# Optimization experiments

Hardware: AMD Instinct MI355X
Metric: run time of the kernel (lower is better)

Reference implementation:

```python
import jax, jax.numpy as jnp
import numpy as np

D_HEAD = 128
H_Q = 16
H_K = 4
D_MODEL = 2048
B = 2
T = 2048


def setup_inputs() -> dict:
    key = jax.random.key(0)
    k1, k2, k3, k4, k5 = jax.random.split(key, 5)
    s = 0.02
    return {
        "x": jax.random.normal(k1, (B, T, D_MODEL), dtype=jnp.float32),
        "wq": jax.random.normal(k2, (D_HEAD * H_Q, D_MODEL), dtype=jnp.float32) * s,
        "wk": jax.random.normal(k3, (D_HEAD * H_K, D_MODEL), dtype=jnp.float32) * s,
        "wv": jax.random.normal(k4, (D_HEAD * H_K, D_MODEL), dtype=jnp.float32) * s,
        "wo": jax.random.normal(k5, (D_MODEL, D_HEAD * H_Q), dtype=jnp.float32) * s,
    }


def reference(x, wq, wk, wv, wo):
    Bs, Ts, _ = x.shape
    g = H_Q // H_K  # query groups per kv head
    # projections (torch Linear: y = x @ W^T)
    Q = (x @ wq.T).reshape(Bs, Ts, H_Q, D_HEAD).transpose(0, 2, 1, 3)  # [B,hq,T,d]
    K = (x @ wk.T).reshape(Bs, Ts, H_K, D_HEAD).transpose(0, 2, 1, 3)  # [B,hk,T,d]
    V = (x @ wv.T).reshape(Bs, Ts, H_K, D_HEAD).transpose(0, 2, 1, 3)  # [B,hk,T,d]
    Qg = Q.reshape(Bs, g, H_K, Ts, D_HEAD)  # [B,g,hk,T,d]
    scale = D_HEAD ** -0.5
    attn = jnp.einsum("bghtd,bhsd->bghts", Qg, K) * scale  # [B,g,hk,T,T]
    causal = jnp.tril(jnp.ones((Ts, Ts), dtype=bool))
    attn = jnp.where(causal, attn, -jnp.inf)
    attn = jax.nn.softmax(attn, axis=-1)
    out = jnp.einsum("bghts,bhsd->bghtd", attn, V)  # [B,g,hk,T,d]
    out = out.reshape(Bs, H_Q, Ts, D_HEAD).transpose(0, 2, 1, 3).reshape(Bs, Ts, H_Q * D_HEAD)
    return out @ wo.T
```

## Files before the change

### kernel.cpp

```cpp
#include <hip/hip_runtime.h>
#include <hip/hip_bf16.h>
#include <stdint.h>

#define DMODEL 2048
#define HQ 16
#define HKV 4
#define DH 128
#define SEQT 2048
#define BATCH 2

typedef __bf16 bf16x8 __attribute__((ext_vector_type(8)));
typedef float f32x4 __attribute__((ext_vector_type(4)));
typedef float f32x16 __attribute__((ext_vector_type(16)));
typedef unsigned short u16x4 __attribute__((ext_vector_type(4)));
typedef unsigned short u16x8 __attribute__((ext_vector_type(8)));

__device__ __forceinline__ unsigned short f2bf(float x) {
  __hip_bfloat16 h = __float2bfloat16(x);
  return __builtin_bit_cast(unsigned short, h);
}
__device__ __forceinline__ unsigned int pack2(float a, float b) {
  return (unsigned int)f2bf(a) | ((unsigned int)f2bf(b) << 16);
}

__device__ __forceinline__ void gload_lds16(const void* g, void* lds) {
  __builtin_amdgcn_global_load_lds(
      (const __attribute__((address_space(1))) void*)(uintptr_t)g,
      (__attribute__((address_space(3))) void*)(uint32_t)(uintptr_t)lds,
      16, 0, 0);
}

__global__ __launch_bounds__(256) void cast_all_kernel(
    const float* __restrict__ x, const float* __restrict__ wq,
    const float* __restrict__ wk, const float* __restrict__ wv,
    const float* __restrict__ wo,
    unsigned short* __restrict__ xb, unsigned short* __restrict__ wqb,
    unsigned short* __restrict__ wkb, unsigned short* __restrict__ wvb,
    unsigned short* __restrict__ wob) {
  int i = blockIdx.x * 256 + threadIdx.x;
  const float* in; unsigned short* out; int off;
  if (i < 1048576)      { in = x;  out = xb;  off = i; }
  else if (i < 1572864) { in = wq; out = wqb; off = i - 1048576; }
  else if (i < 1703936) { in = wk; out = wkb; off = i - 1572864; }
  else if (i < 1835008) { in = wv; out = wvb; off = i - 1703936; }
  else                  { in = wo; out = wob; off = i - 1835008; }
  const float4* p = reinterpret_cast<const float4*>(in) + (size_t)off * 2;
  float4 a = p[0], b = p[1];
  u16x8 o;
  o[0] = f2bf(a.x); o[1] = f2bf(a.y); o[2] = f2bf(a.z); o[3] = f2bf(a.w);
  o[4] = f2bf(b.x); o[5] = f2bf(b.y); o[6] = f2bf(b.z); o[7] = f2bf(b.w);
  *(reinterpret_cast<u16x8*>(out) + off) = o;
}

template <bool OUT_BF16>
__device__ __forceinline__ void gemm_body(
    unsigned short* As, unsigned short* Bs,
    const unsigned short* __restrict__ A, const unsigned short* __restrict__ B,
    void* __restrict__ Cv, int N, int K, int row0, int col0) {
  const int tid = threadIdx.x;
  const int wave = tid >> 6, lane = tid & 63;
  const int wr = (wave >> 1) * 64, wc = (wave & 1) * 64;
  const int l15 = lane & 15, l4 = lane >> 4;
  const int srow = wave * 32 + (lane >> 2);
  const int scol = (lane & 3) * 8;

  f32x4 acc[4][4] = {};

  for (int k0 = 0; k0 < K; k0 += 64) {
#pragma unroll
    for (int h = 0; h < 2; ++h) {
      const unsigned short* gA = A + (size_t)(row0 + srow) * K + k0 + h * 32 + scol;
      gload_lds16(gA, (char*)As + h * 8192 + wave * 2048);
      gload_lds16(gA + (size_t)16 * K, (char*)As + h * 8192 + wave * 2048 + 1024);
      const unsigned short* gB = B + (size_t)(col0 + srow) * K + k0 + h * 32 + scol;
      gload_lds16(gB, (char*)Bs + h * 8192 + wave * 2048);
      gload_lds16(gB + (size_t)16 * K, (char*)Bs + h * 8192 + wave * 2048 + 1024);
    }
    __syncthreads();

    bf16x8 af[2][4], bfr[2][4];
#pragma unroll
    for (int h = 0; h < 2; ++h)
#pragma unroll
      for (int i = 0; i < 4; ++i) {
        af[h][i]  = *reinterpret_cast<const bf16x8*>(&As[h * 4096 + (wr + i * 16 + l15) * 32 + l4 * 8]);
        bfr[h][i] = *reinterpret_cast<const bf16x8*>(&Bs[h * 4096 + (wc + i * 16 + l15) * 32 + l4 * 8]);
      }
#pragma unroll
    for (int h = 0; h < 2; ++h)
#pragma unroll
      for (int i = 0; i < 4; ++i)
#pragma unroll
        for (int j = 0; j < 4; ++j)
          acc[i][j] = __builtin_amdgcn_mfma_f32_16x16x32_bf16(af[h][i], bfr[h][j], acc[i][j], 0, 0, 0);
    __syncthreads();
  }

#pragma unroll
  for (int i = 0; i < 4; ++i) {
    const int rrow = row0 + wr + i * 16 + l4 * 4;
#pragma unroll
    for (int j = 0; j < 4; ++j) {
      const int ccol = col0 + wc + j * 16 + l15;
#pragma unroll
      for (int r = 0; r < 4; ++r) {
        const size_t idx = (size_t)(rrow + r) * N + ccol;
        if constexpr (OUT_BF16)
          ((unsigned short*)Cv)[idx] = f2bf(acc[i][j][r]);
        else
          ((float*)Cv)[idx] = acc[i][j][r];
      }
    }
  }
}

template <bool OUT_BF16>
__global__ __launch_bounds__(256) void gemm_bt(
    const unsigned short* __restrict__ A, const unsigned short* __restrict__ B,
    void* __restrict__ Cv, int N, int K) {
  __shared__ alignas(16) unsigned short As[2][128 * 32];
  __shared__ alignas(16) unsigned short Bs[2][128 * 32];
  gemm_body<OUT_BF16>(&As[0][0], &Bs[0][0], A, B, Cv, N, K,
                      blockIdx.x * 128, blockIdx.y * 128);
}

__global__ __launch_bounds__(256) void gemm_kv(
    const unsigned short* __restrict__ xb, const unsigned short* __restrict__ wkb,
    const unsigned short* __restrict__ wvb,
    unsigned short* __restrict__ Kb, unsigned short* __restrict__ VTb) {
  __shared__ alignas(16) unsigned short As[2][128 * 32];
  __shared__ alignas(16) unsigned short Bs[2][128 * 32];
  const int bid = blockIdx.x;
  if (bid < 128) {
    const int tx = bid >> 2, ty = bid & 3;
    gemm_body<true>(&As[0][0], &Bs[0][0], xb, wkb, Kb, 512, DMODEL,
                    tx * 128, ty * 128);
  } else {
    const int lb = bid - 128;
    const int tz = lb & 1, ty = (lb >> 1) & 15, tx = lb >> 5;
    gemm_body<true>(&As[0][0], &Bs[0][0], wvb,
                    xb + (size_t)tz * SEQT * DMODEL,
                    VTb + (size_t)tz * 512 * SEQT, SEQT, DMODEL,
                    tx * 128, ty * 128);
  }
}

__global__ __launch_bounds__(256, 2) void attn_kernel(
    const unsigned short* __restrict__ Q, const unsigned short* __restrict__ Kc,
    const unsigned short* __restrict__ VT, unsigned short* __restrict__ AO) {
  __shared__ alignas(16) unsigned short Ks[2][16 * 512];
  __shared__ alignas(16) unsigned short Vs[2][16 * 512];

  const int tid = threadIdx.x;
  const int wave = tid >> 6, lane = tid & 63;
  const int bid = blockIdx.x;
  const int round = bid >> 8, pairslot = bid & 255;
  const int bhk = pairslot & 7;
  const int jp = pairslot >> 3;
  const int j = round ? jp : 63 - jp;
  const int b = bhk >> 2, hk = bhk & 3;
  const int h = hk + wave * 4;
  const int q0 = j * 32;
  const int jt = j >> 1;
  const int lq = lane & 31, hi = lane >> 5;
  const float SCL2E = 0.1275174473f;

  const size_t qrow = (size_t)(b * SEQT + q0 + lq);
  const unsigned short* qp = Q + qrow * (HQ * DH) + h * DH + hi * 8;
  bf16x8 qf[8];
#pragma unroll
  for (int dc = 0; dc < 8; ++dc)
    qf[dc] = *reinterpret_cast<const bf16x8*>(qp + dc * 16);

  f32x16 acc_o[4] = {};
  float mrun = -INFINITY, lrun = 0.f;

  const unsigned short* kbase = Kc + (size_t)b * SEQT * (HKV * DH) + hk * DH;
  const unsigned short* vtb = VT + ((size_t)b * (HKV * DH) + hk * DH) * SEQT;

  auto STAGE = [&](int buf, int kvb2) {
#pragma unroll
    for (int i = 0; i < 4; ++i) {
      const int f = i * 4 + wave;
      const int sub = f >> 3, dc = f & 7;
      const unsigned short* g = kbase + (size_t)(kvb2 + sub * 32 + lq) * (HKV * DH) + dc * 16 + hi * 8;
      gload_lds16(g, (char*)Ks[buf] + f * 1024);
    }
#pragma unroll
    for (int i = 0; i < 4; ++i) {
      const int f = i * 4 + wave;
      const int dt = f >> 2, ks = f & 3;
      const unsigned short* g = vtb + (size_t)(dt * 32 + lq) * SEQT + kvb2 + ks * 16 + hi * 8;
      gload_lds16(g, (char*)Vs[buf] + f * 1024);
    }
  };

  STAGE(0, 0);
  __syncthreads();
  int cur = 0;

  for (int t = 0; t <= jt; ++t) {
    if (t < jt) STAGE(cur ^ 1, (t + 1) * 64);
    const int kvb = t * 64;
    const bool s1v = (kvb + 32 <= q0);
    const bool d0 = (kvb == q0), d1 = (kvb + 32 == q0);

    f32x16 st0 = {}, st1 = {};
    __builtin_amdgcn_s_setprio(1);
#pragma unroll
    for (int dc = 0; dc < 8; ++dc) {
      bf16x8 kf = *reinterpret_cast<const bf16x8*>((char*)Ks[cur] + dc * 1024 + lane * 16);
      st0 = __builtin_amdgcn_mfma_f32_32x32x16_bf16(kf, qf[dc], st0, 0, 0, 0);
    }
    if (s1v) {
#pragma unroll
      for (int dc = 0; dc < 8; ++dc) {
        bf16x8 kf = *reinterpret_cast<const bf16x8*>((char*)Ks[cur] + (8 + dc) * 1024 + lane * 16);
        st1 = __builtin_amdgcn_mfma_f32_32x32x16_bf16(kf, qf[dc], st1, 0, 0, 0);
      }
    }
    __builtin_amdgcn_s_setprio(0);

    float p0[16], p1[16];
    float tmax = -INFINITY;
#pragma unroll
    for (int r = 0; r < 16; ++r) {
      const int srw = (r & 3) + 8 * (r >> 2) + 4 * hi;
      float v = st0[r] * SCL2E;
      if (d0 && srw > lq) v = -INFINITY;
      p0[r] = v; tmax = fmaxf(tmax, v);
    }
    if (s1v) {
#pragma unroll
      for (int r = 0; r < 16; ++r) {
        const int srw = (r & 3) + 8 * (r >> 2) + 4 * hi;
        float v = st1[r] * SCL2E;
        if (d1 && srw > lq) v = -INFINITY;
        p1[r] = v; tmax = fmaxf(tmax, v);
      }
    }
    tmax = fmaxf(tmax, __shfl_xor(tmax, 32));
    if (!__all(tmax <= mrun)) {
      const float mnew = fmaxf(mrun, tmax);
      const float fsc = __builtin_amdgcn_exp2f(mrun - mnew);
      lrun *= fsc;
#pragma unroll
      for (int dt = 0; dt < 4; ++dt)
#pragma unroll
        for (int r = 0; r < 16; ++r) acc_o[dt][r] *= fsc;
      mrun = mnew;
    }
    float psum = 0.f;
#pragma unroll
    for (int r = 0; r < 16; ++r) { p0[r] = __builtin_amdgcn_exp2f(p0[r] - mrun); psum += p0[r]; }
    if (s1v) {
#pragma unroll
      for (int r = 0; r < 16; ++r) { p1[r] = __builtin_amdgcn_exp2f(p1[r] - mrun); psum += p1[r]; }
    }
    psum += __shfl_xor(psum, 32);
    lrun += psum;

    union { unsigned int u[4]; bf16x8 v; } pf0, pf1, pf2, pf3;
    {
      unsigned int x0 = pack2(p0[0], p0[1]),  x1 = pack2(p0[2], p0[3]);
      unsigned int x2 = pack2(p0[4], p0[5]),  x3 = pack2(p0[6], p0[7]);
      unsigned int x4 = pack2(p0[8], p0[9]),  x5 = pack2(p0[10], p0[11]);
      unsigned int x6 = pack2(p0[12], p0[13]), x7 = pack2(p0[14], p0[15]);
      unsigned int x0s = __shfl_xor(x0, 32), x1s = __shfl_xor(x1, 32);
      unsigned int x2s = __shfl_xor(x2, 32), x3s = __shfl_xor(x3, 32);
      unsigned int x4s = __shfl_xor(x4, 32), x5s = __shfl_xor(x5, 32);
      unsigned int x6s = __shfl_xor(x6, 32), x7s = __shfl_xor(x7, 32);
      pf0.u[0] = hi ? x2s : x0;  pf0.u[1] = hi ? x3s : x1;
      pf0.u[2] = hi ? x2  : x0s; pf0.u[3] = hi ? x3  : x1s;
      pf1.u[0] = hi ? x6s : x4;  pf1.u[1] = hi ? x7s : x5;
      pf1.u[2] = hi ? x6  : x4s; pf1.u[3] = hi ? x7  : x5s;
    }
    if (s1v) {
      unsigned int x0 = pack2(p1[0], p1[1]),  x1 = pack2(p1[2], p1[3]);
      unsigned int x2 = pack2(p1[4], p1[5]),  x3 = pack2(p1[6], p1[7]);
      unsigned int x4 = pack2(p1[8], p1[9]),  x5 = pack2(p1[10], p1[11]);
      unsigned int x6 = pack2(p1[12], p1[13]), x7 = pack2(p1[14], p1[15]);
      unsigned int x0s = __shfl_xor(x0, 32), x1s = __shfl_xor(x1, 32);
      unsigned int x2s = __shfl_xor(x2, 32), x3s = __shfl_xor(x3, 32);
      unsigned int x4s = __shfl_xor(x4, 32), x5s = __shfl_xor(x5, 32);
      unsigned int x6s = __shfl_xor(x6, 32), x7s = __shfl_xor(x7, 32);
      pf2.u[0] = hi ? x2s : x0;  pf2.u[1] = hi ? x3s : x1;
      pf2.u[2] = hi ? x2  : x0s; pf2.u[3] = hi ? x3  : x1s;
      pf3.u[0] = hi ? x6s : x4;  pf3.u[1] = hi ? x7s : x5;
      pf3.u[2] = hi ? x6  : x4s; pf3.u[3] = hi ? x7  : x5s;
    }

    __builtin_amdgcn_s_setprio(1);
#pragma unroll
    for (int dt = 0; dt < 4; ++dt) {
      bf16x8 v0 = *reinterpret_cast<const bf16x8*>((char*)Vs[cur] + (dt * 4 + 0) * 1024 + lane * 16);
      bf16x8 v1 = *reinterpret_cast<const bf16x8*>((char*)Vs[cur] + (dt * 4 + 1) * 1024 + lane * 16);
      acc_o[dt] = __builtin_amdgcn_mfma_f32_32x32x16_bf16(v0, pf0.v, acc_o[dt], 0, 0, 0);
      acc_o[dt] = __builtin_amdgcn_mfma_f32_32x32x16_bf16(v1, pf1.v, acc_o[dt], 0, 0, 0);
    }
    if (s1v) {
#pragma unroll
      for (int dt = 0; dt < 4; ++dt) {
        bf16x8 v2 = *reinterpret_cast<const bf16x8*>((char*)Vs[cur] + (dt * 4 + 2) * 1024 + lane * 16);
        bf16x8 v3 = *reinterpret_cast<const bf16x8*>((char*)Vs[cur] + (dt * 4 + 3) * 1024 + lane * 16);
        acc_o[dt] = __builtin_amdgcn_mfma_f32_32x32x16_bf16(v2, pf2.v, acc_o[dt], 0, 0, 0);
        acc_o[dt] = __builtin_amdgcn_mfma_f32_32x32x16_bf16(v3, pf3.v, acc_o[dt], 0, 0, 0);
      }
    }
    __builtin_amdgcn_s_setprio(0);
    __syncthreads();
    cur ^= 1;
  }

  const float inv = 1.f / lrun;
  unsigned short* op = AO + qrow * (HQ * DH) + h * DH;
#pragma unroll
  for (int dt = 0; dt < 4; ++dt) {
#pragma unroll
    for (int g2 = 0; g2 < 4; ++g2) {
      u16x4 w;
#pragma unroll
      for (int jj = 0; jj < 4; ++jj) w[jj] = f2bf(acc_o[dt][g2 * 4 + jj] * inv);
      *reinterpret_cast<u16x4*>(op + dt * 32 + g2 * 8 + 4 * hi) = w;
    }
  }
}

extern "C" void kernel_launch(void* const* d_in, const int* in_sizes, int n_in,
                              void* d_out, int out_size, void* d_ws, size_t ws_size,
                              hipStream_t stream) {
  const float* x  = (const float*)d_in[0];
  const float* wq = (const float*)d_in[1];
  const float* wk = (const float*)d_in[2];
  const float* wv = (const float*)d_in[3];
  const float* wo = (const float*)d_in[4];
  float* out = (float*)d_out;

  const size_t N_X  = (size_t)BATCH * SEQT * DMODEL;
  const size_t N_WQ = (size_t)HQ * DH * DMODEL;
  const size_t N_WK = (size_t)HKV * DH * DMODEL;
  const size_t N_Q  = (size_t)BATCH * SEQT * HQ * DH;
  const size_t N_K  = (size_t)BATCH * SEQT * HKV * DH;

  unsigned short* xb  = (unsigned short*)d_ws;
  unsigned short* wqb = xb  + N_X;
  unsigned short* wkb = wqb + N_WQ;
  unsigned short* wvb = wkb + N_WK;
  unsigned short* wob = wvb + N_WK;
  unsigned short* Qb  = wob + N_WQ;
  unsigned short* Kb  = Qb  + N_Q;
  unsigned short* VTb = Kb  + N_K;
  unsigned short* AOb = VTb + N_K;

  cast_all_kernel<<<dim3(9216), dim3(256), 0, stream>>>(
      x, wq, wk, wv, wo, xb, wqb, wkb, wvb, wob);

  gemm_bt<true><<<dim3(32, 16, 1), 256, 0, stream>>>(xb, wqb, Qb, 2048, DMODEL);
  gemm_kv<<<dim3(256), 256, 0, stream>>>(xb, wkb, wvb, Kb, VTb);
  attn_kernel<<<dim3(512, 1, 1), 256, 0, stream>>>(Qb, Kb, VTb, AOb);
  gemm_bt<false><<<dim3(32, 16, 1), 256, 0, stream>>>(AOb, wob, out, 2048, DMODEL);
}
```

Measured before the change: 214.7 us.

## Fuse Q/K/V projections, fold softmax scale into Wq, pair attention query tiles

Merges the Q projection and the K/V projection GEMMs into one launch of 768 blocks, which removes a kernel boundary and improves the tail. The softmax scale and log2(e) factor are folded into Wq during the bf16 cast, so the per-score multiply leaves the attention inner loop. Each attention block now handles a long and a short causal query tile together and reuses every staged K/V tile for both. This halves the grid to 256 blocks and lowers launch bounds to one block per CU, raising register pressure and reducing occupancy. Prescaling Wq before the bf16 cast also changes rounding slightly.

```diff
diff --git a/kernel.cpp b/kernel.cpp
--- a/kernel.cpp
+++ b/kernel.cpp
@@ -38,17 +38,17 @@
     unsigned short* __restrict__ wkb, unsigned short* __restrict__ wvb,
     unsigned short* __restrict__ wob) {
   int i = blockIdx.x * 256 + threadIdx.x;
-  const float* in; unsigned short* out; int off;
+  const float* in; unsigned short* out; int off; float s = 1.0f;
   if (i < 1048576)      { in = x;  out = xb;  off = i; }
-  else if (i < 1572864) { in = wq; out = wqb; off = i - 1048576; }
+  else if (i < 1572864) { in = wq; out = wqb; off = i - 1048576; s = 0.1275174473f; }
   else if (i < 1703936) { in = wk; out = wkb; off = i - 1572864; }
   else if (i < 1835008) { in = wv; out = wvb; off = i - 1703936; }
   else                  { in = wo; out = wob; off = i - 1835008; }
   const float4* p = reinterpret_cast<const float4*>(in) + (size_t)off * 2;
   float4 a = p[0], b = p[1];
   u16x8 o;
-  o[0] = f2bf(a.x); o[1] = f2bf(a.y); o[2] = f2bf(a.z); o[3] = f2bf(a.w);
-  o[4] = f2bf(b.x); o[5] = f2bf(b.y); o[6] = f2bf(b.z); o[7] = f2bf(b.w);
+  o[0] = f2bf(a.x * s); o[1] = f2bf(a.y * s); o[2] = f2bf(a.z * s); o[3] = f2bf(a.w * s);
+  o[4] = f2bf(b.x * s); o[5] = f2bf(b.y * s); o[6] = f2bf(b.z * s); o[7] = f2bf(b.w * s);
   *(reinterpret_cast<u16x8*>(out) + off) = o;
 }
 
@@ -114,6 +114,31 @@
   }
 }
 
+__global__ __launch_bounds__(256) void gemm_qkv(
+    const unsigned short* __restrict__ xb, const unsigned short* __restrict__ wqb,
+    const unsigned short* __restrict__ wkb, const unsigned short* __restrict__ wvb,
+    unsigned short* __restrict__ Qb, unsigned short* __restrict__ Kb,
+    unsigned short* __restrict__ VTb) {
+  __shared__ alignas(16) unsigned short As[2][128 * 32];
+  __shared__ alignas(16) unsigned short Bs[2][128 * 32];
+  const int bid = blockIdx.x;
+  if (bid < 512) {
+    gemm_body<true>(&As[0][0], &Bs[0][0], xb, wqb, Qb, 2048, DMODEL,
+                    (bid >> 4) * 128, (bid & 15) * 128);
+  } else if (bid < 640) {
+    const int r = bid - 512;
+    gemm_body<true>(&As[0][0], &Bs[0][0], xb, wkb, Kb, 512, DMODEL,
+                    (r >> 2) * 128, (r & 3) * 128);
+  } else {
+    const int r = bid - 640;
+    const int tz = r & 1, ty = (r >> 1) & 15, tx = r >> 5;
+    gemm_body<true>(&As[0][0], &Bs[0][0], wvb,
+                    xb + (size_t)tz * SEQT * DMODEL,
+                    VTb + (size_t)tz * 512 * SEQT, SEQT, DMODEL,
+                    tx * 128, ty * 128);
+  }
+}
+
 template <bool OUT_BF16>
 __global__ __launch_bounds__(256) void gemm_bt(
     const unsigned short* __restrict__ A, const unsigned short* __restrict__ B,
@@ -124,28 +149,126 @@
                       blockIdx.x * 128, blockIdx.y * 128);
 }
 
-__global__ __launch_bounds__(256) void gemm_kv(
-    const unsigned short* __restrict__ xb, const unsigned short* __restrict__ wkb,
-    const unsigned short* __restrict__ wvb,
-    unsigned short* __restrict__ Kb, unsigned short* __restrict__ VTb) {
-  __shared__ alignas(16) unsigned short As[2][128 * 32];
-  __shared__ alignas(16) unsigned short Bs[2][128 * 32];
-  const int bid = blockIdx.x;
-  if (bid < 128) {
-    const int tx = bid >> 2, ty = bid & 3;
-    gemm_body<true>(&As[0][0], &Bs[0][0], xb, wkb, Kb, 512, DMODEL,
-                    tx * 128, ty * 128);
-  } else {
-    const int lb = bid - 128;
-    const int tz = lb & 1, ty = (lb >> 1) & 15, tx = lb >> 5;
-    gemm_body<true>(&As[0][0], &Bs[0][0], wvb,
-                    xb + (size_t)tz * SEQT * DMODEL,
-                    VTb + (size_t)tz * 512 * SEQT, SEQT, DMODEL,
-                    tx * 128, ty * 128);
-  }
-}
-
-__global__ __launch_bounds__(256, 2) void attn_kernel(
+__device__ __forceinline__ void tile_pass(
+    const char* ksb, const char* vsb, int lane, int hi, int lq,
+    int kvb, int q0, const bf16x8* qf, f32x16* acc, float& mrun, float& lrun) {
+  const bool s1v = (kvb + 32 <= q0);
+  const bool d0 = (kvb == q0), d1 = (kvb + 32 == q0);
+
+  f32x16 st0 = {}, st1 = {};
+  __builtin_amdgcn_s_setprio(1);
+#pragma unroll
+  for (int dc = 0; dc < 8; ++dc) {
+    bf16x8 kf = *reinterpret_cast<const bf16x8*>(ksb + dc * 1024 + lane * 16);
+    st0 = __builtin_amdgcn_mfma_f32_32x32x16_bf16(kf, qf[dc], st0, 0, 0, 0);
+  }
+  if (s1v) {
+#pragma unroll
+    for (int dc = 0; dc < 8; ++dc) {
+      bf16x8 kf = *reinterpret_cast<const bf16x8*>(ksb + (8 + dc) * 1024 + lane * 16);
+      st1 = __builtin_amdgcn_mfma_f32_32x32x16_bf16(kf, qf[dc], st1, 0, 0, 0);
+    }
+  }
+  __builtin_amdgcn_s_setprio(0);
+
+  float p0[16], p1[16];
+#pragma unroll
+  for (int r = 0; r < 16; ++r) p0[r] = st0[r];
+  if (d0) {
+#pragma unroll
+    for (int r = 0; r < 16; ++r) {
+      const int srw = (r & 3) + 8 * (r >> 2) + 4 * hi;
+      if (srw > lq) p0[r] = -INFINITY;
+    }
+  }
+  float tmax = -INFINITY;
+#pragma unroll
+  for (int r = 0; r < 16; ++r) tmax = fmaxf(tmax, p0[r]);
+  if (s1v) {
+#pragma unroll
+    for (int r = 0; r < 16; ++r) p1[r] = st1[r];
+    if (d1) {
+#pragma unroll
+      for (int r = 0; r < 16; ++r) {
+        const int srw = (r & 3) + 8 * (r >> 2) + 4 * hi;
+        if (srw > lq) p1[r] = -INFINITY;
+      }
+    }
+#pragma unroll
+    for (int r = 0; r < 16; ++r) tmax = fmaxf(tmax, p1[r]);
+  }
+  tmax = fmaxf(tmax, __shfl_xor(tmax, 32));
+  if (!__all(tmax <= mrun)) {
+    const float mnew = fmaxf(mrun, tmax);
+    const float fsc = __builtin_amdgcn_exp2f(mrun - mnew);
+    lrun *= fsc;
+#pragma unroll
+    for (int dt = 0; dt < 4; ++dt)
+#pragma unroll
+      for (int r = 0; r < 16; ++r) acc[dt][r] *= fsc;
+    mrun = mnew;
+  }
+  float psum = 0.f;
+#pragma unroll
+  for (int r = 0; r < 16; ++r) { p0[r] = __builtin_amdgcn_exp2f(p0[r] - mrun); psum += p0[r]; }
+  if (s1v) {
+#pragma unroll
+    for (int r = 0; r < 16; ++r) { p1[r] = __builtin_amdgcn_exp2f(p1[r] - mrun); psum += p1[r]; }
+  }
+  psum += __shfl_xor(psum, 32);
+  lrun += psum;
+
+  union { unsigned int u[4]; bf16x8 v; } pf0, pf1, pf2, pf3;
+  {
+    unsigned int x0 = pack2(p0[0], p0[1]),  x1 = pack2(p0[2], p0[3]);
+    unsigned int x2 = pack2(p0[4], p0[5]),  x3 = pack2(p0[6], p0[7]);
+    unsigned int x4 = pack2(p0[8], p0[9]),  x5 = pack2(p0[10], p0[11]);
+    unsigned int x6 = pack2(p0[12], p0[13]), x7 = pack2(p0[14], p0[15]);
+    unsigned int x0s = __shfl_xor(x0, 32), x1s = __shfl_xor(x1, 32);
+    unsigned int x2s = __shfl_xor(x2, 32), x3s = __shfl_xor(x3, 32);
+    unsigned int x4s = __shfl_xor(x4, 32), x5s = __shfl_xor(x5, 32);
+    unsigned int x6s = __shfl_xor(x6, 32), x7s = __shfl_xor(x7, 32);
+    pf0.u[0] = hi ? x2s : x0;  pf0.u[1] = hi ? x3s : x1;
+    pf0.u[2] = hi ? x2  : x0s; pf0.u[3] = hi ? x3  : x1s;
+    pf1.u[0] = hi ? x6s : x4;  pf1.u[1] = hi ? x7s : x5;
+    pf1.u[2] = hi ? x6  : x4s; pf1.u[3] = hi ? x7  : x5s;
+  }
+  if (s1v) {
+    unsigned int x0 = pack2(p1[0], p1[1]),  x1 = pack2(p1[2], p1[3]);
+    unsigned int x2 = pack2(p1[4], p1[5]),  x3 = pack2(p1[6], p1[7]);
+    unsigned int x4 = pack2(p1[8], p1[9]),  x5 = pack2(p1[10], p1[11]);
+    unsigned int x6 = pack2(p1[12], p1[13]), x7 = pack2(p1[14], p1[15]);
+    unsigned int x0s = __shfl_xor(x0, 32), x1s = __shfl_xor(x1, 32);
+    unsigned int x2s = __shfl_xor(x2, 32), x3s = __shfl_xor(x3, 32);
+    unsigned int x4s = __shfl_xor(x4, 32), x5s = __shfl_xor(x5, 32);
+    unsigned int x6s = __shfl_xor(x6, 32), x7s = __shfl_xor(x7, 32);
+    pf2.u[0] = hi ? x2s : x0;  pf2.u[1] = hi ? x3s : x1;
+    pf2.u[2] = hi ? x2  : x0s; pf2.u[3] = hi ? x3  : x1s;
+    pf3.u[0] = hi ? x6s : x4;  pf3.u[1] = hi ? x7s : x5;
+    pf3.u[2] = hi ? x6  : x4s; pf3.u[3] = hi ? x7  : x5s;
+  }
+
+  __builtin_amdgcn_s_setprio(1);
+#pragma unroll
+  for (int dt = 0; dt < 4; ++dt) {
+    bf16x8 v0 = *reinterpret_cast<const bf16x8*>(vsb + (dt * 4 + 0) * 1024 + lane * 16);
+    bf16x8 v1 = *reinterpret_cast<const bf16x8*>(vsb + (dt * 4 + 1) * 1024 + lane * 16);
+    acc[dt] = __builtin_amdgcn_mfma_f32_32x32x16_bf16(v0, pf0.v, acc[dt], 0, 0, 0);
+    acc[dt] = __builtin_amdgcn_mfma_f32_32x32x16_bf16(v1, pf1.v, acc[dt], 0, 0, 0);
+  }
+  if (s1v) {
+#pragma unroll
+    for (int dt = 0; dt < 4; ++dt) {
+      bf16x8 v2 = *reinterpret_cast<const bf16x8*>(vsb + (dt * 4 + 2) * 1024 + lane * 16);
+      bf16x8 v3 = *reinterpret_cast<const bf16x8*>(vsb + (dt * 4 + 3) * 1024 + lane * 16);
+      acc[dt] = __builtin_amdgcn_mfma_f32_32x32x16_bf16(v2, pf2.v, acc[dt], 0, 0, 0);
+      acc[dt] = __builtin_amdgcn_mfma_f32_32x32x16_bf16(v3, pf3.v, acc[dt], 0, 0, 0);
+    }
+  }
+  __builtin_amdgcn_s_setprio(0);
+}
+
+__global__ __launch_bounds__(256, 1) void attn_kernel(
     const unsigned short* __restrict__ Q, const unsigned short* __restrict__ Kc,
     const unsigned short* __restrict__ VT, unsigned short* __restrict__ AO) {
   __shared__ alignas(16) unsigned short Ks[2][16 * 512];
@@ -154,26 +277,30 @@
   const int tid = threadIdx.x;
   const int wave = tid >> 6, lane = tid & 63;
   const int bid = blockIdx.x;
-  const int round = bid >> 8, pairslot = bid & 255;
-  const int bhk = pairslot & 7;
-  const int jp = pairslot >> 3;
-  const int j = round ? jp : 63 - jp;
+  const int bhk = bid & 7;
+  const int pairidx = bid >> 3;
   const int b = bhk >> 2, hk = bhk & 3;
   const int h = hk + wave * 4;
-  const int q0 = j * 32;
-  const int jt = j >> 1;
+  const int jl = 63 - pairidx, js = pairidx;
+  const int q0l = jl * 32, q0s = js * 32;
+  const int jtl = jl >> 1, jts = js >> 1;
   const int lq = lane & 31, hi = lane >> 5;
-  const float SCL2E = 0.1275174473f;
-
-  const size_t qrow = (size_t)(b * SEQT + q0 + lq);
-  const unsigned short* qp = Q + qrow * (HQ * DH) + h * DH + hi * 8;
-  bf16x8 qf[8];
-#pragma unroll
-  for (int dc = 0; dc < 8; ++dc)
-    qf[dc] = *reinterpret_cast<const bf16x8*>(qp + dc * 16);
-
-  f32x16 acc_o[4] = {};
-  float mrun = -INFINITY, lrun = 0.f;
+
+  const size_t qrowL = (size_t)(b * SEQT + q0l + lq);
+  const size_t qrowS = (size_t)(b * SEQT + q0s + lq);
+  bf16x8 qfL[8], qfS[8];
+  {
+    const unsigned short* qpL = Q + qrowL * (HQ * DH) + h * DH + hi * 8;
+    const unsigned short* qpS = Q + qrowS * (HQ * DH) + h * DH + hi * 8;
+#pragma unroll
+    for (int dc = 0; dc < 8; ++dc) {
+      qfL[dc] = *reinterpret_cast<const bf16x8*>(qpL + dc * 16);
+      qfS[dc] = *reinterpret_cast<const bf16x8*>(qpS + dc * 16);
+    }
+  }
+
+  f32x16 accL[4] = {}, accS[4] = {};
+  float mL = -INFINITY, lL = 0.f, mS = -INFINITY, lS = 0.f;
 
   const unsigned short* kbase = Kc + (size_t)b * SEQT * (HKV * DH) + hk * DH;
   const unsigned short* vtb = VT + ((size_t)b * (HKV * DH) + hk * DH) * SEQT;
@@ -199,131 +326,33 @@
   __syncthreads();
   int cur = 0;
 
-  for (int t = 0; t <= jt; ++t) {
-    if (t < jt) STAGE(cur ^ 1, (t + 1) * 64);
-    const int kvb = t * 64;
-    const bool s1v = (kvb + 32 <= q0);
-    const bool d0 = (kvb == q0), d1 = (kvb + 32 == q0);
-
-    f32x16 st0 = {}, st1 = {};
-    __builtin_amdgcn_s_setprio(1);
-#pragma unroll
-    for (int dc = 0; dc < 8; ++dc) {
-      bf16x8 kf = *reinterpret_cast<const bf16x8*>((char*)Ks[cur] + dc * 1024 + lane * 16);
-      st0 = __builtin_amdgcn_mfma_f32_32x32x16_bf16(kf, qf[dc], st0, 0, 0, 0);
-    }
-    if (s1v) {
-#pragma unroll
-      for (int dc = 0; dc < 8; ++dc) {
-        bf16x8 kf = *reinterpret_cast<const bf16x8*>((char*)Ks[cur] + (8 + dc) * 1024 + lane * 16);
-        st1 = __builtin_amdgcn_mfma_f32_32x32x16_bf16(kf, qf[dc], st1, 0, 0, 0);
-      }
-    }
-    __builtin_amdgcn_s_setprio(0);
-
-    float p0[16], p1[16];
-    float tmax = -INFINITY;
-#pragma unroll
-    for (int r = 0; r < 16; ++r) {
-      const int srw = (r & 3) + 8 * (r >> 2) + 4 * hi;
-      float v = st0[r] * SCL2E;
-      if (d0 && srw > lq) v = -INFINITY;
-      p0[r] = v; tmax = fmaxf(tmax, v);
-    }
-    if (s1v) {
-#pragma unroll
-      for (int r = 0; r < 16; ++r) {
-        const int srw = (r & 3) + 8 * (r >> 2) + 4 * hi;
-        float v = st1[r] * SCL2E;
-        if (d1 && srw > lq) v = -INFINITY;
-        p1[r] = v; tmax = fmaxf(tmax, v);
-      }
-    }
-    tmax = fmaxf(tmax, __shfl_xor(tmax, 32));
-    if (!__all(tmax <= mrun)) {
-      const float mnew = fmaxf(mrun, tmax);
-      const float fsc = __builtin_amdgcn_exp2f(mrun - mnew);
-      lrun *= fsc;
-#pragma unroll
-      for (int dt = 0; dt < 4; ++dt)
-#pragma unroll
-        for (int r = 0; r < 16; ++r) acc_o[dt][r] *= fsc;
-      mrun = mnew;
-    }
-    float psum = 0.f;
-#pragma unroll
-    for (int r = 0; r < 16; ++r) { p0[r] = __builtin_amdgcn_exp2f(p0[r] - mrun); psum += p0[r]; }
-    if (s1v) {
-#pragma unroll
-      for (int r = 0; r < 16; ++r) { p1[r] = __builtin_amdgcn_exp2f(p1[r] - mrun); psum += p1[r]; }
-    }
-    psum += __shfl_xor(psum, 32);
-    lrun += psum;
-
-    union { unsigned int u[4]; bf16x8 v; } pf0, pf1, pf2, pf3;
-    {
-      unsigned int x0 = pack2(p0[0], p0[1]),  x1 = pack2(p0[2], p0[3]);
-      unsigned int x2 = pack2(p0[4], p0[5]),  x3 = pack2(p0[6], p0[7]);
-      unsigned int x4 = pack2(p0[8], p0[9]),  x5 = pack2(p0[10], p0[11]);
-      unsigned int x6 = pack2(p0[12], p0[13]), x7 = pack2(p0[14], p0[15]);
-      unsigned int x0s = __shfl_xor(x0, 32), x1s = __shfl_xor(x1, 32);
-      unsigned int x2s = __shfl_xor(x2, 32), x3s = __shfl_xor(x3, 32);
-      unsigned int x4s = __shfl_xor(x4, 32), x5s = __shfl_xor(x5, 32);
-      unsigned int x6s = __shfl_xor(x6, 32), x7s = __shfl_xor(x7, 32);
-      pf0.u[0] = hi ? x2s : x0;  pf0.u[1] = hi ? x3s : x1;
-      pf0.u[2] = hi ? x2  : x0s; pf0.u[3] = hi ? x3  : x1s;
-      pf1.u[0] = hi ? x6s : x4;  pf1.u[1] = hi ? x7s : x5;
-      pf1.u[2] = hi ? x6  : x4s; pf1.u[3] = hi ? x7  : x5s;
-    }
-    if (s1v) {
-      unsigned int x0 = pack2(p1[0], p1[1]),  x1 = pack2(p1[2], p1[3]);
-      unsigned int x2 = pack2(p1[4], p1[5]),  x3 = pack2(p1[6], p1[7]);
-      unsigned int x4 = pack2(p1[8], p1[9]),  x5 = pack2(p1[10], p1[11]);
-      unsigned int x6 = pack2(p1[12], p1[13]), x7 = pack2(p1[14], p1[15]);
-      unsigned int x0s = __shfl_xor(x0, 32), x1s = __shfl_xor(x1, 32);
-      unsigned int x2s = __shfl_xor(x2, 32), x3s = __shfl_xor(x3, 32);
-      unsigned int x4s = __shfl_xor(x4, 32), x5s = __shfl_xor(x5, 32);
-      unsigned int x6s = __shfl_xor(x6, 32), x7s = __shfl_xor(x7, 32);
-      pf2.u[0] = hi ? x2s : x0;  pf2.u[1] = hi ? x3s : x1;
-      pf2.u[2] = hi ? x2  : x0s; pf2.u[3] = hi ? x3  : x1s;
-      pf3.u[0] = hi ? x6s : x4;  pf3.u[1] = hi ? x7s : x5;
-      pf3.u[2] = hi ? x6  : x4s; pf3.u[3] = hi ? x7  : x5s;
-    }
-
-    __builtin_amdgcn_s_setprio(1);
-#pragma unroll
-    for (int dt = 0; dt < 4; ++dt) {
-      bf16x8 v0 = *reinterpret_cast<const bf16x8*>((char*)Vs[cur] + (dt * 4 + 0) * 1024 + lane * 16);
-      bf16x8 v1 = *reinterpret_cast<const bf16x8*>((char*)Vs[cur] + (dt * 4 + 1) * 1024 + lane * 16);
-      acc_o[dt] = __builtin_amdgcn_mfma_f32_32x32x16_bf16(v0, pf0.v, acc_o[dt], 0, 0, 0);
-      acc_o[dt] = __builtin_amdgcn_mfma_f32_32x32x16_bf16(v1, pf1.v, acc_o[dt], 0, 0, 0);
-    }
-    if (s1v) {
-#pragma unroll
-      for (int dt = 0; dt < 4; ++dt) {
-        bf16x8 v2 = *reinterpret_cast<const bf16x8*>((char*)Vs[cur] + (dt * 4 + 2) * 1024 + lane * 16);
-        bf16x8 v3 = *reinterpret_cast<const bf16x8*>((char*)Vs[cur] + (dt * 4 + 3) * 1024 + lane * 16);
-        acc_o[dt] = __builtin_amdgcn_mfma_f32_32x32x16_bf16(v2, pf2.v, acc_o[dt], 0, 0, 0);
-        acc_o[dt] = __builtin_amdgcn_mfma_f32_32x32x16_bf16(v3, pf3.v, acc_o[dt], 0, 0, 0);
-      }
-    }
-    __builtin_amdgcn_s_setprio(0);
+  for (int t = 0; t <= jtl; ++t) {
+    if (t < jtl) STAGE(cur ^ 1, (t + 1) * 64);
+    const char* ksb = (const char*)Ks[cur];
+    const char* vsb = (const char*)Vs[cur];
+    tile_pass(ksb, vsb, lane, hi, lq, t * 64, q0l, qfL, accL, mL, lL);
+    if (t <= jts)
+      tile_pass(ksb, vsb, lane, hi, lq, t * 64, q0s, qfS, accS, mS, lS);
     __syncthreads();
     cur ^= 1;
   }
 
-  const float inv = 1.f / lrun;
-  unsigned short* op = AO + qrow * (HQ * DH) + h * DH;
-#pragma unroll
-  for (int dt = 0; dt < 4; ++dt) {
-#pragma unroll
-    for (int g2 = 0; g2 < 4; ++g2) {
-      u16x4 w;
-#pragma unroll
-      for (int jj = 0; jj < 4; ++jj) w[jj] = f2bf(acc_o[dt][g2 * 4 + jj] * inv);
-      *reinterpret_cast<u16x4*>(op + dt * 32 + g2 * 8 + 4 * hi) = w;
-    }
-  }
+  auto writeO = [&](const f32x16* acc, float lrun, size_t qrow) {
+    const float inv = 1.f / lrun;
+    unsigned short* op = AO + qrow * (HQ * DH) + h * DH;
+#pragma unroll
+    for (int dt = 0; dt < 4; ++dt) {
+#pragma unroll
+      for (int g2 = 0; g2 < 4; ++g2) {
+        u16x4 w;
+#pragma unroll
+        for (int jj = 0; jj < 4; ++jj) w[jj] = f2bf(acc[dt][g2 * 4 + jj] * inv);
+        *reinterpret_cast<u16x4*>(op + dt * 32 + g2 * 8 + 4 * hi) = w;
+      }
+    }
+  };
+  writeO(accL, lL, qrowL);
+  writeO(accS, lS, qrowS);
 }
 
 extern "C" void kernel_launch(void* const* d_in, const int* in_sizes, int n_in,
@@ -355,8 +384,7 @@
   cast_all_kernel<<<dim3(9216), dim3(256), 0, stream>>>(
       x, wq, wk, wv, wo, xb, wqb, wkb, wvb, wob);
 
-  gemm_bt<true><<<dim3(32, 16, 1), 256, 0, stream>>>(xb, wqb, Qb, 2048, DMODEL);
-  gemm_kv<<<dim3(256), 256, 0, stream>>>(xb, wkb, wvb, Kb, VTb);
-  attn_kernel<<<dim3(512, 1, 1), 256, 0, stream>>>(Qb, Kb, VTb, AOb);
+  gemm_qkv<<<dim3(768), 256, 0, stream>>>(xb, wqb, wkb, wvb, Qb, Kb, VTb);
+  attn_kernel<<<dim3(256, 1, 1), 256, 0, stream>>>(Qb, Kb, VTb, AOb);
   gemm_bt<false><<<dim3(32, 16, 1), 256, 0, stream>>>(AOb, wob, out, 2048, DMODEL);
 }
```

Result: no change. 211.1 us (-1.7%).
